# Performance work log

Measured on AMD Instinct MI355X. Metric: run time of the kernel, lower is better.

Reference implementation:

```python
import jax, jax.numpy as jnp
import numpy as np

OUT = 7  # output_size (RoIPool 7x7)


def _crop_one(fm_all, roi, K):
    """Adaptive max-pool one ROI to [C, OUT, OUT].

    fm_all: [B, C, H, W]; roi: [5] int32 (batch, x1, y1, x2, y2).
    K: static max bin extent (ceil(H/OUT)+1), covers any ROI size.
    Matches torch adaptive_max_pool2d bins: start=floor(i*n/OUT), end=ceil((i+1)*n/OUT).
    """
    H, W = fm_all.shape[2], fm_all.shape[3]
    b, x1, y1, x2, y2 = roi[0], roi[1], roi[2], roi[3], roi[4]
    fm = jnp.take(fm_all, b, axis=0)  # [C, H, W]
    h = y2 - y1
    w = x2 - x1
    o = jnp.arange(OUT)
    ys = y1 + (o * h) // OUT
    ye = y1 + ((o + 1) * h + OUT - 1) // OUT  # ceil div
    xs = x1 + (o * w) // OUT
    xe = x1 + ((o + 1) * w + OUT - 1) // OUT
    k = jnp.arange(K)

    # --- pool along width (separable rectangle max) ---
    col_idx = jnp.clip(xs[:, None] + k[None, :], 0, W - 1)   # [OUT, K]
    col_valid = k[None, :] < (xe - xs)[:, None]              # [OUT, K]
    g = fm[:, :, col_idx]                                    # [C, H, OUT, K]
    g = jnp.where(col_valid, g, -jnp.inf)
    tw = g.max(axis=-1)                                      # [C, H, OUT]

    # --- pool along height ---
    row_idx = jnp.clip(ys[:, None] + k[None, :], 0, H - 1)   # [OUT, K]
    row_valid = k[None, :] < (ye - ys)[:, None]
    g2 = tw[:, row_idx, :]                                   # [C, OUT, K, OUT]
    g2 = jnp.where(row_valid[None, :, :, None], g2, -jnp.inf)
    return g2.max(axis=2)                                    # [C, OUT, OUT]


def setup_inputs() -> dict:
    key = jax.random.key(0)
    B, C, H, W, R = 2, 256, 50, 50, 192
    feature_map = jax.random.normal(key, (B, C, H, W), dtype=jnp.float32)
    rng = np.random.default_rng(0)
    batch = rng.integers(0, B, R)
    x1 = rng.integers(0, W - 1, R)
    x2 = rng.integers(x1 + 1, W + 1)  # ensure x2 > x1, <= W
    y1 = rng.integers(0, H - 1, R)
    y2 = rng.integers(y1 + 1, H + 1)
    rois = jnp.asarray(np.stack([batch, x1, y1, x2, y2], axis=1).astype(np.int32))
    return {"feature_map": feature_map, "rois": rois}


def reference(feature_map, rois):
    H = feature_map.shape[2]
    K = -(-H // OUT) + 1  # static max bin extent
    return jax.vmap(_crop_one, in_axes=(None, 0, None))(feature_map, rois, K)  # [R, C, OUT, OUT]
```

## Files before the change

### kernel.cpp

```cpp
#include <hip/hip_runtime.h>
#include <math.h>


#define OUT_N 7
#define WPB 4
#define CHW 4
#define CPB (WPB * CHW)
#define LDSW 66

__global__ __launch_bounds__(256, 5) void roicrop_kernel(
    const float* __restrict__ fm,
    const int* __restrict__ rois,
    float* __restrict__ out,
    int R, int C, int H, int W, int nfm)
{
    __shared__ float tw[CPB][OUT_N][LDSW];

    const int lane = threadIdx.x & 63;
    const int wave = threadIdx.x >> 6;
    const int cg_per_r = C / CPB;
    const int r  = blockIdx.x / cg_per_r;
    const int cg = blockIdx.x - r * cg_per_r;

    const int csub = lane >> 4;
    const int l2   = lane & 15;
    const int c    = cg * CPB + wave * CHW + csub;
    const int wc   = wave * CHW + csub;

    const int* roi = rois + r * 5;
    const int b  = roi[0];
    const int x1 = roi[1];
    const int y1 = roi[2];
    const int x2 = roi[3];
    const int y2 = roi[4];
    const int h = y2 - y1;
    const int w = x2 - x1;

    const int x0  = x1 & ~1;
    const int off = x1 - x0;
    const unsigned base = (unsigned)(b * C + c) * (unsigned)(H * W)
                        + (unsigned)(x0 + 2 * l2);
    const unsigned lim  = (unsigned)(nfm - 2);

    int ys[OUT_N], ym[OUT_N];
    int KB = 1;
    #pragma unroll
    for (int i = 0; i < OUT_N; ++i) {
        ys[i] = y1 + (i * h) / OUT_N;
        const int ye = y1 + ((i + 1) * h + OUT_N - 1) / OUT_N;
        ym[i] = ye - 1;
        const int hb = ye - ys[i];
        KB = hb > KB ? hb : KB;
    }

    const int npass = (off + w > 32) ? 2 : 1;

    for (int p = 0; p < npass; ++p) {
        const unsigned pb = base + (unsigned)(32 * p);

        float2 m[OUT_N];
        #pragma unroll
        for (int i = 0; i < OUT_N; ++i) m[i] = make_float2(-INFINITY, -INFINITY);

        for (int k = 0; k < KB; ++k) {
            float2 v[OUT_N];
            #pragma unroll
            for (int i = 0; i < OUT_N; ++i) {
                int row = ys[i] + k;
                if (row > ym[i]) row = ym[i];
                unsigned ia = pb + (unsigned)(row * W);
                if (ia > lim) ia = lim;
                v[i] = *reinterpret_cast<const float2*>(fm + ia);
            }
            #pragma unroll
            for (int i = 0; i < OUT_N; ++i) {
                m[i].x = fmaxf(m[i].x, v[i].x);
                m[i].y = fmaxf(m[i].y, v[i].y);
            }
        }

        #pragma unroll
        for (int i = 0; i < OUT_N; ++i) {
            *reinterpret_cast<float2*>(&tw[wc][i][32 * p + 2 * l2]) = m[i];
        }
    }
    __syncthreads();

    float* obase = out + ((size_t)r * C + cg * CPB) * (OUT_N * OUT_N);
    for (int o = threadIdx.x; o < CPB * OUT_N * OUT_N; o += 256) {
        const int twc = o / (OUT_N * OUT_N);
        const int l   = o - twc * (OUT_N * OUT_N);
        const int i   = l / OUT_N;
        const int j   = l - i * OUT_N;
        const int xs  = (j * w) / OUT_N;
        const int xe  = ((j + 1) * w + OUT_N - 1) / OUT_N;
        float m2 = -INFINITY;
        for (int dx = xs; dx < xe; ++dx) {
            m2 = fmaxf(m2, tw[twc][i][off + dx]);
        }
        obase[o] = m2;
    }
}

extern "C" void kernel_launch(void* const* d_in, const int* in_sizes, int n_in,
                              void* d_out, int out_size, void* d_ws, size_t ws_size,
                              hipStream_t stream)
{
    const float* fm = (const float*)d_in[0];
    const int* rois = (const int*)d_in[1];
    float* out      = (float*)d_out;

    const int R = in_sizes[1] / 5;
    const int C = out_size / (R * OUT_N * OUT_N);
    const int H = 50;
    const int W = 50;
    const int nfm = in_sizes[0];

    const int grid = R * (C / CPB);
    roicrop_kernel<<<grid, 256, 0, stream>>>(fm, rois, out, R, C, H, W, nfm);
}
```

Before: 73.59 us.

## Double-buffer row loads in ROI max-pool and shrink LDS for higher occupancy

The row-reduction loop now software-pipelines global loads across two register buffers, so the next rows' loads are issued before the current rows are reduced. The trip count is rounded up to an even number; the extra row is clamped to the bin end, so results stay correct. The LDS row width drops from 66 to 54 and writes past slot 52 are guarded, which allows the launch-bounds hint to rise from 5 to 6 blocks per CU. The double buffer raises register pressure against the higher occupancy target and may cause spills.

```diff
diff --git a/kernel.cpp b/kernel.cpp
--- a/kernel.cpp
+++ b/kernel.cpp
@@ -6,9 +6,9 @@
 #define WPB 4
 #define CHW 4
 #define CPB (WPB * CHW)
-#define LDSW 66
+#define LDSW 54
 
-__global__ __launch_bounds__(256, 5) void roicrop_kernel(
+__global__ __launch_bounds__(256, 6) void roicrop_kernel(
     const float* __restrict__ fm,
     const int* __restrict__ rois,
     float* __restrict__ out,
@@ -52,36 +52,56 @@
         const int hb = ye - ys[i];
         KB = hb > KB ? hb : KB;
     }
+    const int KB2 = (KB + 1) & ~1;
 
     const int npass = (off + w > 32) ? 2 : 1;
 
     for (int p = 0; p < npass; ++p) {
         const unsigned pb = base + (unsigned)(32 * p);
 
+        #define LOADG(dst, g)                                              \
+            {                                                              \
+                _Pragma("unroll")                                          \
+                for (int i = 0; i < OUT_N; ++i) {                          \
+                    int row = ys[i] + (g);                                 \
+                    if (row > ym[i]) row = ym[i];                          \
+                    unsigned ia = pb + (unsigned)(row * W);                \
+                    if (ia > lim) ia = lim;                                \
+                    (dst)[i] = *reinterpret_cast<const float2*>(fm + ia);  \
+                }                                                          \
+            }
+        #define REDUCE(src)                                                \
+            {                                                              \
+                _Pragma("unroll")                                          \
+                for (int i = 0; i < OUT_N; ++i) {                          \
+                    m[i].x = fmaxf(m[i].x, (src)[i].x);                    \
+                    m[i].y = fmaxf(m[i].y, (src)[i].y);                    \
+                }                                                          \
+            }
+
         float2 m[OUT_N];
         #pragma unroll
         for (int i = 0; i < OUT_N; ++i) m[i] = make_float2(-INFINITY, -INFINITY);
 
-        for (int k = 0; k < KB; ++k) {
-            float2 v[OUT_N];
-            #pragma unroll
-            for (int i = 0; i < OUT_N; ++i) {
-                int row = ys[i] + k;
-                if (row > ym[i]) row = ym[i];
-                unsigned ia = pb + (unsigned)(row * W);
-                if (ia > lim) ia = lim;
-                v[i] = *reinterpret_cast<const float2*>(fm + ia);
-            }
-            #pragma unroll
-            for (int i = 0; i < OUT_N; ++i) {
-                m[i].x = fmaxf(m[i].x, v[i].x);
-                m[i].y = fmaxf(m[i].y, v[i].y);
-            }
+        float2 vA[OUT_N], vB[OUT_N];
+        LOADG(vA, 0)
+        LOADG(vB, 1)
+        for (int k = 0; k < KB2; k += 2) {
+            const bool more = (k + 2 < KB2);
+            REDUCE(vA);
+            if (more) LOADG(vA, k + 2)
+            REDUCE(vB);
+            if (more) LOADG(vB, k + 3)
         }
+        #undef LOADG
+        #undef REDUCE
 
         #pragma unroll
         for (int i = 0; i < OUT_N; ++i) {
-            *reinterpret_cast<float2*>(&tw[wc][i][32 * p + 2 * l2]) = m[i];
+            const int slot = 32 * p + 2 * l2;
+            if (slot < 52) {
+                *reinterpret_cast<float2*>(&tw[wc][i][slot]) = m[i];
+            }
         }
     }
     __syncthreads();
```

New measurement: 74.28 us. No clear change (+0.9%).
